# Kernel optimization log

Hardware: AMD Instinct MI355X
Metric: run time of the kernel (lower is better)

## Reference

```python
import jax, jax.numpy as jnp
import numpy as np

K = 8  # num_neighbors
EPS = 1e-12

def _l2_normalize(x):
    n = jnp.sqrt(jnp.sum(x * x, axis=1, keepdims=True))
    return x / jnp.maximum(n, EPS)

def setup_inputs() -> dict:
    key = jax.random.key(0)
    k1, k2, k3, k4 = jax.random.split(key, 4)
    feats = jax.random.normal(k1, (1024, 2048), dtype=jnp.float32)
    bank_features = jax.random.normal(k2, (2048, 2048), dtype=jnp.float32)
    logits = jax.random.normal(k3, (2048, 1000), dtype=jnp.float32)
    bank_probs = jax.nn.softmax(logits, axis=1)  # bank stores softmaxed probs
    image_bank = jax.random.normal(k4, (2048, 3, 224, 224), dtype=jnp.float32)
    return {"feats": feats, "bank_features": bank_features,
            "bank_probs": bank_probs, "image_bank": image_bank}

def reference(feats, bank_features, bank_probs, image_bank):
    # cosine distances: [N, Q]
    dist = 1.0 - _l2_normalize(feats) @ _l2_normalize(bank_features).T
    # original code: topk(largest=True) on distances -> keep faithful
    _, idxs = jax.lax.top_k(dist, K)            # idxs: [N, K]
    grads = jnp.mean(bank_features[idxs], axis=1)   # [N, D]
    pred_probs = jnp.mean(bank_probs[idxs], axis=1)  # [N, C]
    # mean over K neighbor images; loop over small fixed K to avoid a
    # [N, K, 3, 224, 224] (~5 GB) intermediate (torch avoids it by chunking N)
    acc = image_bank[idxs[:, 0]]
    for k in range(1, K):
        acc = acc + image_bank[idxs[:, k]]
    pred_images = acc / K                            # [N, 3, 224, 224]
    pred_labels = jnp.argmax(pred_probs, axis=1)     # [N]
    return pred_labels, pred_probs, pred_images, grads
```

## Files before the change

kernel.cpp:

```cpp
#include <hip/hip_runtime.h>
#include <math.h>

#define NF   1024
#define NB   2048
#define DIM  2048
#define NC   1000
#define IMG  150528
#define IMG4 37632
#define KSEL 8

typedef float f32x4 __attribute__((ext_vector_type(4)));
typedef float f32x2 __attribute__((ext_vector_type(2)));

__global__ __launch_bounds__(256) void norms_kernel(
    const float* __restrict__ feats, const float* __restrict__ bank,
    float* __restrict__ invf, float* __restrict__ invb)
{
    int row = blockIdx.x;
    const float* src;
    float* dst;
    if (row < NF) { src = feats + (size_t)row * DIM; dst = invf + row; }
    else          { src = bank  + (size_t)(row - NF) * DIM; dst = invb + (row - NF); }

    float s = 0.f;
    for (int c = threadIdx.x; c < DIM / 4; c += 256) {
        float4 v = ((const float4*)src)[c];
        s += v.x * v.x + v.y * v.y + v.z * v.z + v.w * v.w;
    }
    __shared__ float red[4];
    for (int off = 32; off; off >>= 1) s += __shfl_down(s, off, 64);
    if ((threadIdx.x & 63) == 0) red[threadIdx.x >> 6] = s;
    __syncthreads();
    if (threadIdx.x == 0) {
        float t = red[0] + red[1] + red[2] + red[3];
        float n = fmaxf(sqrtf(t), 1e-12f);
        *dst = 1.0f / n;
    }
}

#define GBM 128
#define GBN 64
#define GBK 16

__global__ __launch_bounds__(256) void dist_kernel(
    const float* __restrict__ A, const float* __restrict__ B,
    const float* __restrict__ invf, const float* __restrict__ invb,
    float* __restrict__ dist)
{
    __shared__ float As[2][GBK][GBM];
    __shared__ float Bs[2][GBK][GBN];

    const int tid  = threadIdx.x;
    const int brow = blockIdx.y * GBM;
    const int bcol = blockIdx.x * GBN;
    const int ty   = tid >> 4;
    const int tx   = tid & 15;

    const int lrow = tid >> 2;
    const int lk   = (tid & 3) * 4;

    f32x2 acc01[8] = {};
    f32x2 acc23[8] = {};

    {
        float4 a0 = *(const float4*)(A + (size_t)(brow + lrow)      * DIM + lk);
        float4 a1 = *(const float4*)(A + (size_t)(brow + lrow + 64) * DIM + lk);
        float4 b0 = *(const float4*)(B + (size_t)(bcol + lrow)      * DIM + lk);
        As[0][lk + 0][lrow] = a0.x; As[0][lk + 1][lrow] = a0.y;
        As[0][lk + 2][lrow] = a0.z; As[0][lk + 3][lrow] = a0.w;
        As[0][lk + 0][lrow + 64] = a1.x; As[0][lk + 1][lrow + 64] = a1.y;
        As[0][lk + 2][lrow + 64] = a1.z; As[0][lk + 3][lrow + 64] = a1.w;
        Bs[0][lk + 0][lrow] = b0.x; Bs[0][lk + 1][lrow] = b0.y;
        Bs[0][lk + 2][lrow] = b0.z; Bs[0][lk + 3][lrow] = b0.w;
    }
    __syncthreads();

    int cur = 0;
    for (int k0 = 0; k0 < DIM; k0 += GBK) {
        const bool has_next = (k0 + GBK) < DIM;
        float4 na0, na1, nb0;
        if (has_next) {
            na0 = *(const float4*)(A + (size_t)(brow + lrow)      * DIM + k0 + GBK + lk);
            na1 = *(const float4*)(A + (size_t)(brow + lrow + 64) * DIM + k0 + GBK + lk);
            nb0 = *(const float4*)(B + (size_t)(bcol + lrow)      * DIM + k0 + GBK + lk);
        }

        #pragma unroll
        for (int k = 0; k < GBK; ++k) {
            float4 av0 = *(const float4*)&As[cur][k][ty * 8];
            float4 av1 = *(const float4*)&As[cur][k][ty * 8 + 4];
            f32x2 b01 = *(const f32x2*)&Bs[cur][k][tx * 4];
            f32x2 b23 = *(const f32x2*)&Bs[cur][k][tx * 4 + 2];
            float a[8] = {av0.x, av0.y, av0.z, av0.w, av1.x, av1.y, av1.z, av1.w};
            #pragma unroll
            for (int i = 0; i < 8; ++i) {
                f32x2 ai = {a[i], a[i]};
                acc01[i] = __builtin_elementwise_fma(ai, b01, acc01[i]);
                acc23[i] = __builtin_elementwise_fma(ai, b23, acc23[i]);
            }
        }

        if (has_next) {
            const int nxt = cur ^ 1;
            As[nxt][lk + 0][lrow] = na0.x; As[nxt][lk + 1][lrow] = na0.y;
            As[nxt][lk + 2][lrow] = na0.z; As[nxt][lk + 3][lrow] = na0.w;
            As[nxt][lk + 0][lrow + 64] = na1.x; As[nxt][lk + 1][lrow + 64] = na1.y;
            As[nxt][lk + 2][lrow + 64] = na1.z; As[nxt][lk + 3][lrow + 64] = na1.w;
            Bs[nxt][lk + 0][lrow] = nb0.x; Bs[nxt][lk + 1][lrow] = nb0.y;
            Bs[nxt][lk + 2][lrow] = nb0.z; Bs[nxt][lk + 3][lrow] = nb0.w;
        }
        __syncthreads();
        cur ^= 1;
    }

    float fi[8], fb[4];
    #pragma unroll
    for (int i = 0; i < 8; ++i) fi[i] = invf[brow + ty * 8 + i];
    #pragma unroll
    for (int j = 0; j < 4; ++j) fb[j] = invb[bcol + tx * 4 + j];
    #pragma unroll
    for (int i = 0; i < 8; ++i) {
        size_t ro = (size_t)(brow + ty * 8 + i) * NB + bcol + tx * 4;
        float4 o;
        o.x = 1.0f - acc01[i].x * fi[i] * fb[0];
        o.y = 1.0f - acc01[i].y * fi[i] * fb[1];
        o.z = 1.0f - acc23[i].x * fi[i] * fb[2];
        o.w = 1.0f - acc23[i].y * fi[i] * fb[3];
        *(float4*)(dist + ro) = o;
    }
}

__global__ __launch_bounds__(256) void topk_kernel(
    const float* __restrict__ dist, int* __restrict__ idxs)
{
    __shared__ float v[NB];
    __shared__ float rv[256];
    __shared__ int   ri[256];
    int row = blockIdx.x;
    const float* src = dist + (size_t)row * NB;
    for (int c = threadIdx.x; c < NB; c += 256) v[c] = src[c];
    __syncthreads();

    for (int sel = 0; sel < KSEL; ++sel) {
        float bv = -1e30f; int bi = NB;
        for (int c = threadIdx.x; c < NB; c += 256) {
            float x = v[c];
            if (x > bv) { bv = x; bi = c; }
        }
        rv[threadIdx.x] = bv; ri[threadIdx.x] = bi;
        __syncthreads();
        for (int s = 128; s; s >>= 1) {
            if (threadIdx.x < s) {
                float ov = rv[threadIdx.x + s]; int oi = ri[threadIdx.x + s];
                if (ov > rv[threadIdx.x] ||
                    (ov == rv[threadIdx.x] && oi < ri[threadIdx.x])) {
                    rv[threadIdx.x] = ov; ri[threadIdx.x] = oi;
                }
            }
            __syncthreads();
        }
        if (threadIdx.x == 0) { idxs[row * KSEL + sel] = ri[0]; v[ri[0]] = -1e30f; }
        __syncthreads();
    }
}

__global__ __launch_bounds__(256) void probs_kernel(
    const float* __restrict__ bank_probs, const int* __restrict__ idxs,
    float* __restrict__ out_labels, float* __restrict__ out_probs)
{
    int row = blockIdx.x;
    __shared__ int id[KSEL];
    if (threadIdx.x < KSEL) id[threadIdx.x] = idxs[row * KSEL + threadIdx.x];
    __syncthreads();

    float bv = -1e30f; int bc = NC;
    for (int c = threadIdx.x; c < NC; c += 256) {
        float s = 0.f;
        #pragma unroll
        for (int k = 0; k < KSEL; ++k) s += bank_probs[(size_t)id[k] * NC + c];
        s *= (1.0f / KSEL);
        out_probs[(size_t)row * NC + c] = s;
        if (s > bv) { bv = s; bc = c; }
    }
    __shared__ float rv[256];
    __shared__ int   ri[256];
    rv[threadIdx.x] = bv; ri[threadIdx.x] = bc;
    __syncthreads();
    for (int s = 128; s; s >>= 1) {
        if (threadIdx.x < s) {
            float ov = rv[threadIdx.x + s]; int oi = ri[threadIdx.x + s];
            if (ov > rv[threadIdx.x] ||
                (ov == rv[threadIdx.x] && oi < ri[threadIdx.x])) {
                rv[threadIdx.x] = ov; ri[threadIdx.x] = oi;
            }
        }
        __syncthreads();
    }
    if (threadIdx.x == 0) out_labels[row] = (float)ri[0];
}

__global__ __launch_bounds__(256) void grads_kernel(
    const float* __restrict__ bank, const int* __restrict__ idxs,
    float* __restrict__ out_grads)
{
    int row = blockIdx.x;
    __shared__ int id[KSEL];
    if (threadIdx.x < KSEL) id[threadIdx.x] = idxs[row * KSEL + threadIdx.x];
    __syncthreads();
    for (int c = threadIdx.x; c < DIM / 4; c += 256) {
        float4 acc = {0.f, 0.f, 0.f, 0.f};
        #pragma unroll
        for (int k = 0; k < KSEL; ++k) {
            float4 t = ((const float4*)(bank + (size_t)id[k] * DIM))[c];
            acc.x += t.x; acc.y += t.y; acc.z += t.z; acc.w += t.w;
        }
        float4 o = {acc.x * 0.125f, acc.y * 0.125f, acc.z * 0.125f, acc.w * 0.125f};
        ((float4*)(out_grads + (size_t)row * DIM))[c] = o;
    }
}

#define ITILES 147
#define RPB    4

__global__ __launch_bounds__(256) void images_kernel(
    const float* __restrict__ image_bank, const int* __restrict__ idxs,
    float* __restrict__ out_images)
{
    const int bid  = blockIdx.x;
    const int tile = bid / (NF / RPB);
    const int rem  = bid % (NF / RPB);
    const int row0 = rem * RPB;
    const int base4 = tile * 256 + threadIdx.x;

    const int* __restrict__ ip = idxs + row0 * KSEL;
    const f32x4* __restrict__ bank4 = (const f32x4*)image_bank;

    f32x4 t[RPB][KSEL];
    #pragma unroll
    for (int r = 0; r < RPB; ++r)
        #pragma unroll
        for (int k = 0; k < KSEL; ++k)
            t[r][k] = bank4[(size_t)ip[r * KSEL + k] * IMG4 + base4];
    __builtin_amdgcn_sched_barrier(0);

    #pragma unroll
    for (int r = 0; r < RPB; ++r) {
        f32x4 s01 = t[r][0] + t[r][1];
        f32x4 s23 = t[r][2] + t[r][3];
        f32x4 s45 = t[r][4] + t[r][5];
        f32x4 s67 = t[r][6] + t[r][7];
        f32x4 o = ((s01 + s23) + (s45 + s67)) * 0.125f;
        f32x4* outp = (f32x4*)(out_images + (size_t)(row0 + r) * IMG) + base4;
        __builtin_nontemporal_store(o, outp);
    }
}

extern "C" void kernel_launch(void* const* d_in, const int* in_sizes, int n_in,
                              void* d_out, int out_size, void* d_ws, size_t ws_size,
                              hipStream_t stream)
{
    const float* feats      = (const float*)d_in[0];
    const float* bank_feats = (const float*)d_in[1];
    const float* bank_probs = (const float*)d_in[2];
    const float* image_bank = (const float*)d_in[3];

    float* out = (float*)d_out;
    float* out_labels = out;
    float* out_probs  = out + NF;
    float* out_images = out + NF + (size_t)NF * NC;
    float* out_grads  = out + NF + (size_t)NF * NC + (size_t)NF * IMG;

    float* dist = out_images;

    float* invf = (float*)d_ws;
    float* invb = invf + NF;
    int*   idxs = (int*)(invb + NB);

    norms_kernel<<<NF + NB, 256, 0, stream>>>(feats, bank_feats, invf, invb);

    dim3 ggrid(NB / GBN, NF / GBM);
    dist_kernel<<<ggrid, 256, 0, stream>>>(feats, bank_feats, invf, invb, dist);

    topk_kernel<<<NF, 256, 0, stream>>>(dist, idxs);

    probs_kernel<<<NF, 256, 0, stream>>>(bank_probs, idxs, out_labels, out_probs);

    grads_kernel<<<NF, 256, 0, stream>>>(bank_feats, idxs, out_grads);

    images_kernel<<<ITILES * (NF / RPB), 256, 0, stream>>>(image_bank, idxs, out_images);
}
```

Measured before the change: 795.5 us.

## Fuse per-tile top-k selection into distance GEMM epilogue

The GEMM epilogue now stages each 128x64 distance tile in shared memory, and each of 128 threads keeps a sorted top-8 for its row over the tile's 64 columns. Per-tile candidates are written to workspace, and a new final kernel reduces the 256 candidates per row to the top 8. This removes the 8 MB distance matrix write/read and the 8-pass argmax over 2048 columns per row. In exchange it adds 33 KB of shared memory per block, which may lower GEMM occupancy, and a serial per-thread insertion sort in the epilogue. The B-tile shared load is also merged into a single float4 read.

```diff
diff --git a/kernel.cpp b/kernel.cpp
--- a/kernel.cpp
+++ b/kernel.cpp
@@ -41,14 +41,16 @@
 #define GBM 128
 #define GBN 64
 #define GBK 16
+#define NCB (NB / GBN)
 
 __global__ __launch_bounds__(256) void dist_kernel(
     const float* __restrict__ A, const float* __restrict__ B,
     const float* __restrict__ invf, const float* __restrict__ invb,
-    float* __restrict__ dist)
+    float* __restrict__ candv, int* __restrict__ candi)
 {
     __shared__ float As[2][GBK][GBM];
     __shared__ float Bs[2][GBK][GBN];
+    __shared__ float ep[GBM][GBN + 1];
 
     const int tid  = threadIdx.x;
     const int brow = blockIdx.y * GBM;
@@ -89,8 +91,9 @@
         for (int k = 0; k < GBK; ++k) {
             float4 av0 = *(const float4*)&As[cur][k][ty * 8];
             float4 av1 = *(const float4*)&As[cur][k][ty * 8 + 4];
-            f32x2 b01 = *(const f32x2*)&Bs[cur][k][tx * 4];
-            f32x2 b23 = *(const f32x2*)&Bs[cur][k][tx * 4 + 2];
+            float4 bv  = *(const float4*)&Bs[cur][k][tx * 4];
+            f32x2 b01 = {bv.x, bv.y};
+            f32x2 b23 = {bv.z, bv.w};
             float a[8] = {av0.x, av0.y, av0.z, av0.w, av1.x, av1.y, av1.z, av1.w};
             #pragma unroll
             for (int i = 0; i < 8; ++i) {
@@ -120,46 +123,68 @@
     for (int j = 0; j < 4; ++j) fb[j] = invb[bcol + tx * 4 + j];
     #pragma unroll
     for (int i = 0; i < 8; ++i) {
-        size_t ro = (size_t)(brow + ty * 8 + i) * NB + bcol + tx * 4;
-        float4 o;
-        o.x = 1.0f - acc01[i].x * fi[i] * fb[0];
-        o.y = 1.0f - acc01[i].y * fi[i] * fb[1];
-        o.z = 1.0f - acc23[i].x * fi[i] * fb[2];
-        o.w = 1.0f - acc23[i].y * fi[i] * fb[3];
-        *(float4*)(dist + ro) = o;
-    }
-}
-
-__global__ __launch_bounds__(256) void topk_kernel(
-    const float* __restrict__ dist, int* __restrict__ idxs)
-{
-    __shared__ float v[NB];
+        ep[ty * 8 + i][tx * 4 + 0] = 1.0f - acc01[i].x * fi[i] * fb[0];
+        ep[ty * 8 + i][tx * 4 + 1] = 1.0f - acc01[i].y * fi[i] * fb[1];
+        ep[ty * 8 + i][tx * 4 + 2] = 1.0f - acc23[i].x * fi[i] * fb[2];
+        ep[ty * 8 + i][tx * 4 + 3] = 1.0f - acc23[i].y * fi[i] * fb[3];
+    }
+    __syncthreads();
+
+    if (tid < GBM) {
+        float lv[KSEL];
+        int   li[KSEL];
+        #pragma unroll
+        for (int s = 0; s < KSEL; ++s) { lv[s] = -1e30f; li[s] = NB; }
+        for (int c = 0; c < GBN; ++c) {
+            float v = ep[tid][c];
+            if (v > lv[KSEL - 1]) {
+                lv[KSEL - 1] = v; li[KSEL - 1] = bcol + c;
+                #pragma unroll
+                for (int p = KSEL - 1; p > 0; --p) {
+                    if (lv[p] > lv[p - 1]) {
+                        float tv = lv[p]; lv[p] = lv[p - 1]; lv[p - 1] = tv;
+                        int   ti = li[p]; li[p] = li[p - 1]; li[p - 1] = ti;
+                    }
+                }
+            }
+        }
+        size_t base = ((size_t)(brow + tid) * NCB + blockIdx.x) * KSEL;
+        #pragma unroll
+        for (int s = 0; s < KSEL; ++s) {
+            candv[base + s] = lv[s];
+            candi[base + s] = li[s];
+        }
+    }
+}
+
+__global__ __launch_bounds__(256) void final_topk_kernel(
+    const float* __restrict__ candv, const int* __restrict__ candi,
+    int* __restrict__ idxs)
+{
+    const int row = blockIdx.x;
+    const int t = threadIdx.x;
+    __shared__ float cv[256];
+    __shared__ int   ci[256];
     __shared__ float rv[256];
     __shared__ int   ri[256];
-    int row = blockIdx.x;
-    const float* src = dist + (size_t)row * NB;
-    for (int c = threadIdx.x; c < NB; c += 256) v[c] = src[c];
+    cv[t] = candv[(size_t)row * 256 + t];
+    ci[t] = candi[(size_t)row * 256 + t];
     __syncthreads();
 
     for (int sel = 0; sel < KSEL; ++sel) {
-        float bv = -1e30f; int bi = NB;
-        for (int c = threadIdx.x; c < NB; c += 256) {
-            float x = v[c];
-            if (x > bv) { bv = x; bi = c; }
-        }
-        rv[threadIdx.x] = bv; ri[threadIdx.x] = bi;
+        rv[t] = cv[t]; ri[t] = ci[t];
         __syncthreads();
         for (int s = 128; s; s >>= 1) {
-            if (threadIdx.x < s) {
-                float ov = rv[threadIdx.x + s]; int oi = ri[threadIdx.x + s];
-                if (ov > rv[threadIdx.x] ||
-                    (ov == rv[threadIdx.x] && oi < ri[threadIdx.x])) {
-                    rv[threadIdx.x] = ov; ri[threadIdx.x] = oi;
+            if (t < s) {
+                float ov = rv[t + s]; int oi = ri[t + s];
+                if (ov > rv[t] || (ov == rv[t] && oi < ri[t])) {
+                    rv[t] = ov; ri[t] = oi;
                 }
             }
             __syncthreads();
         }
-        if (threadIdx.x == 0) { idxs[row * KSEL + sel] = ri[0]; v[ri[0]] = -1e30f; }
+        if (t == 0) idxs[row * KSEL + sel] = ri[0];
+        if (cv[t] == rv[0] && ci[t] == ri[0]) cv[t] = -1e30f;
         __syncthreads();
     }
 }
@@ -270,18 +295,18 @@
     float* out_images = out + NF + (size_t)NF * NC;
     float* out_grads  = out + NF + (size_t)NF * NC + (size_t)NF * IMG;
 
-    float* dist = out_images;
-
-    float* invf = (float*)d_ws;
-    float* invb = invf + NF;
-    int*   idxs = (int*)(invb + NB);
+    float* invf  = (float*)d_ws;
+    float* invb  = invf + NF;
+    int*   idxs  = (int*)(invb + NB);
+    float* candv = (float*)(idxs + NF * KSEL);
+    int*   candi = (int*)(candv + (size_t)NF * NCB * KSEL);
 
     norms_kernel<<<NF + NB, 256, 0, stream>>>(feats, bank_feats, invf, invb);
 
-    dim3 ggrid(NB / GBN, NF / GBM);
-    dist_kernel<<<ggrid, 256, 0, stream>>>(feats, bank_feats, invf, invb, dist);
-
-    topk_kernel<<<NF, 256, 0, stream>>>(dist, idxs);
+    dim3 ggrid(NCB, NF / GBM);
+    dist_kernel<<<ggrid, 256, 0, stream>>>(feats, bank_feats, invf, invb, candv, candi);
+
+    final_topk_kernel<<<NF, 256, 0, stream>>>(candv, candi, idxs);
 
     probs_kernel<<<NF, 256, 0, stream>>>(bank_probs, idxs, out_labels, out_probs);
 
```

Result: no change. 802.6 us (+0.9%).
